# Kernel tuning notes

Measured on AMD Instinct MI355X. Metric: run time of the kernel, lower is better.

## Reference

```python
import jax, jax.numpy as jnp
import numpy as np

KERNEL = 7  # median blur window size (odd)


def setup_inputs() -> dict:
    key = jax.random.key(0)
    # NCHW image batch, values in [0,1) like normalized images
    img = jax.random.uniform(key, (8, 3, 512, 512), dtype=jnp.float32)
    return {"img": img}


def _median_blur(img, k):
    # Matches kornia.filters.median_blur: zero padding ('same'), then median
    # over the k*k window. k*k is odd so the exact middle of the sorted
    # window equals torch.median's lower median.
    pad = k // 2
    b, c, h, w = img.shape
    x = jnp.pad(img, ((0, 0), (0, 0), (pad, pad), (pad, pad)))  # zero pad
    # unfold: [B, C, k*k, H, W] — same materialization as kornia's conv2d
    # with binary one-hot kernels. Loop is over the fixed k*k = 49 taps.
    patches = jnp.stack(
        [x[:, :, i:i + h, j:j + w] for i in range(k) for j in range(k)],
        axis=2,
    )
    mid = (k * k) // 2
    return jnp.sort(patches, axis=2)[:, :, mid]  # [B, C, H, W]


def reference(img):
    return _median_blur(img, KERNEL)
```

## Files before the change

### kernel.cpp

```cpp
#include <hip/hip_runtime.h>
#include <utility>

#define IMG_H 512
#define IMG_W 512

typedef _Float16 h2 __attribute__((ext_vector_type(2)));

__device__ __forceinline__ h2 h2min(h2 a, h2 b) { return __builtin_elementwise_min(a, b); }
__device__ __forceinline__ h2 h2max(h2 a, h2 b) { return __builtin_elementwise_max(a, b); }

struct Op { int kind, a, b; };
constexpr int NSLOT = 352;
constexpr int MAXOPS = 4096;
struct Prog { Op ops[MAXOPS]; int n; int nphys; bool ok; };

constexpr int pow2ceil(int x) { int p = 1; while (p < x) p += p; return p; }

struct Builder {
    Op ops[MAXOPS] = {};
    int n = 0;
    bool pad[NSLOT] = {};
    bool init[NSLOT] = {};
    bool ok = true;

    constexpr void emit(int k, int a, int b) {
        if (n < MAXOPS) ops[n++] = Op{k, a, b}; else ok = false;
    }
    constexpr void load(int s, int c) { emit(2, s, c); pad[s] = false; init[s] = true; }
    constexpr void mov(int d, int s) {
        if (!init[s] || d == s) ok = false;
        emit(1, d, s); pad[d] = pad[s]; init[d] = true;
    }
    constexpr void mkpad(int s) { pad[s] = true; init[s] = true; }
    constexpr void ce_(int a, int b) {
        if (!init[a] || !init[b]) { ok = false; return; }
        if (pad[a] && pad[b]) return;
        if (!pad[a] && pad[b]) return;
        if (pad[a] && !pad[b]) {
            emit(1, a, b); pad[a] = false; pad[b] = true; return;
        }
        emit(0, a, b);
    }
    constexpr void maxin(int a, int b) {
        if (!init[a] || !init[b] || pad[a] || pad[b]) ok = false;
        emit(5, a, b);
    }
    constexpr void minin(int a, int b) {
        if (!init[a] || !init[b] || pad[a] || pad[b]) ok = false;
        emit(4, a, b);
    }
    constexpr void sort_run(int base, int len) {
        for (int p = 1; p < len; p += p)
            for (int k = p; k > 0; k /= 2)
                for (int j = k % p; j + k < len; j += k + k)
                    for (int i = 0; i < k; ++i)
                        if (i + j + k < len)
                            if ((i + j) / (p + p) == (i + j + k) / (p + p))
                                ce_(base + i + j, base + i + j + k);
    }
    constexpr void merge_stage(int base, int P) {
        int nn = 2 * P, p = P;
        for (int k = p; k > 0; k /= 2)
            for (int j = k % p; j + k < nn; j += k + k)
                for (int i = 0; i < k; ++i) {
                    int a = i + j, b = i + j + k;
                    if (b < nn && a / (p + p) == b / (p + p)) ce_(base + a, base + b);
                }
    }
    constexpr void load_col(int base, int c) {
        for (int r = 0; r < 7; ++r) load(base + r, c * 7 + r);
        sort_run(base, 7);
    }
    constexpr void place(int dst, int src, int len, int P) {
        for (int i = 0; i < len; ++i) mov(dst + i, src + i);
        for (int i = len; i < P; ++i) mkpad(dst + i);
    }
    constexpr void merge_to(int dst, int s1, int l1, int s2, int l2) {
        int P = pow2ceil(l1 > l2 ? l1 : l2);
        place(dst, s1, l1, P);
        place(dst + P, s2, l2, P);
        merge_stage(dst, P);
    }
    constexpr void select_med49(int T, int A, int B, int o) {
        for (int t = 0; t < 7; ++t) {
            mov(T + t, A + 17 + t);
            maxin(B + 6 - t, T + t);
        }
        mov(T + 7, A + 24);
        minin(T, T + 1); minin(T + 2, T + 3);
        minin(T + 4, T + 5); minin(T + 6, T + 7);
        minin(T, T + 2); minin(T + 4, T + 6);
        minin(T, T + 4);
        if (!init[T] || pad[T]) ok = false;
        emit(3, o, T);
    }
};

constexpr Prog build() {
    Builder b{};
    constexpr int M12 = 112, M34 = 128, M56 = 144, M78 = 160, M910 = 176, M1112 = 192;
    constexpr int C28A = 208, C28B = 240, C42 = 272, T0 = 336, T1 = 344;

    for (int c = 1; c <= 8; ++c) b.load_col(8 * c, c);
    b.merge_to(M34, 8 * 3, 7, 8 * 4, 7);
    b.merge_to(M56, 8 * 5, 7, 8 * 6, 7);
    b.merge_to(C28A, M34, 14, M56, 14);
    b.merge_to(M12, 8 * 1, 7, 8 * 2, 7);
    b.merge_to(M78, 8 * 7, 7, 8 * 8, 7);

    b.merge_to(C42, C28A, 28, M12, 14);
    b.load_col(8 * 0, 0);
    b.select_med49(T0, C42, 8 * 0, 0);
    b.select_med49(T1, C42, 8 * 7, 1);

    b.merge_to(C42, C28A, 28, M78, 14);
    b.load_col(8 * 9, 9);
    b.select_med49(T0, C42, 8 * 2, 2);
    b.select_med49(T1, C42, 8 * 9, 3);

    b.load_col(8 * 10, 10);
    b.merge_to(M910, 8 * 9, 7, 8 * 10, 7);
    b.merge_to(C28B, M78, 14, M910, 14);

    b.merge_to(C42, C28B, 28, M56, 14);
    b.select_med49(T0, C42, 8 * 4, 4);
    b.load_col(8 * 11, 11);
    b.select_med49(T1, C42, 8 * 11, 5);

    b.load_col(8 * 12, 12);
    b.merge_to(M1112, 8 * 11, 7, 8 * 12, 7);
    b.merge_to(C42, C28B, 28, M1112, 14);
    b.select_med49(T0, C42, 8 * 6, 6);
    b.load_col(8 * 13, 13);
    b.select_med49(T1, C42, 8 * 13, 7);

    Prog p{};
    bool needed[NSLOT] = {};
    int kindr[MAXOPS] = {};
    bool keep[MAXOPS] = {};
    for (int t = b.n - 1; t >= 0; --t) {
        Op o = b.ops[t];
        if (o.kind == 3) { keep[t] = true; kindr[t] = 3; needed[o.b] = true; }
        else if (o.kind == 0) {
            bool na = needed[o.a], nb = needed[o.b];
            if (na && nb)      { keep[t] = true; kindr[t] = 0; }
            else if (na)       { keep[t] = true; kindr[t] = 4; needed[o.b] = true; }
            else if (nb)       { keep[t] = true; kindr[t] = 5; needed[o.a] = true; }
        } else if (o.kind == 1) {
            if (needed[o.a]) { keep[t] = true; kindr[t] = 1; needed[o.a] = false; needed[o.b] = true; }
        } else if (o.kind == 2) {
            if (needed[o.a]) { keep[t] = true; kindr[t] = 2; needed[o.a] = false; }
        } else if (o.kind == 4) {
            if (needed[o.a]) { keep[t] = true; kindr[t] = 4; needed[o.b] = true; }
        } else if (o.kind == 5) {
            if (needed[o.b]) { keep[t] = true; kindr[t] = 5; needed[o.a] = true; }
        }
    }
    p.n = 0;
    for (int t = 0; t < b.n; ++t)
        if (keep[t]) { p.ops[p.n] = b.ops[t]; p.ops[p.n].kind = kindr[t]; ++p.n; }
    p.ok = b.ok;

    bool live[NSLOT] = {};
    bool lu_a[MAXOPS] = {};
    bool lu_b[MAXOPS] = {};
    for (int t = p.n - 1; t >= 0; --t) {
        Op o = p.ops[t];
        if (o.kind == 0 || o.kind == 4 || o.kind == 5) {
            lu_a[t] = !live[o.a]; lu_b[t] = !live[o.b];
        } else if (o.kind == 1 || o.kind == 3) {
            lu_b[t] = !live[o.b];
        }
        if (o.kind == 0) { live[o.a] = false; live[o.b] = false; }
        else if (o.kind == 1 || o.kind == 2 || o.kind == 4) live[o.a] = false;
        else if (o.kind == 5) live[o.b] = false;
        if (o.kind == 0 || o.kind == 4 || o.kind == 5) { live[o.a] = true; live[o.b] = true; }
        else if (o.kind == 1 || o.kind == 3) live[o.b] = true;
    }
    for (int t = 0; t < p.n; ++t) {
        Op o = p.ops[t];
        if (o.kind == 0 && (lu_a[t] || lu_b[t])) p.ok = false;
        if (o.kind == 4 && lu_a[t]) p.ok = false;
        if (o.kind == 5 && lu_b[t]) p.ok = false;
    }
    int phys[NSLOT] = {};
    bool bound[NSLOT] = {};
    int freelist[NSLOT] = {};
    int nfree = 0, nphys = 0;
    for (int t = 0; t < p.n; ++t) {
        Op o = p.ops[t];
        if (o.kind == 0) {
            if (!bound[o.a] || !bound[o.b]) p.ok = false;
            p.ops[t].a = phys[o.a]; p.ops[t].b = phys[o.b];
        } else if (o.kind == 4) {
            if (!bound[o.a] || !bound[o.b]) p.ok = false;
            p.ops[t].a = phys[o.a]; p.ops[t].b = phys[o.b];
            if (lu_b[t]) { freelist[nfree++] = phys[o.b]; bound[o.b] = false; }
        } else if (o.kind == 5) {
            if (!bound[o.a] || !bound[o.b]) p.ok = false;
            p.ops[t].a = phys[o.a]; p.ops[t].b = phys[o.b];
            if (lu_a[t]) { freelist[nfree++] = phys[o.a]; bound[o.a] = false; }
        } else if (o.kind == 1) {
            if (!bound[o.b]) p.ok = false;
            int pb = phys[o.b];
            p.ops[t].b = pb;
            if (lu_b[t]) { freelist[nfree++] = pb; bound[o.b] = false; }
            if (bound[o.a]) { freelist[nfree++] = phys[o.a]; bound[o.a] = false; }
            int pa = (nfree > 0) ? freelist[--nfree] : nphys++;
            phys[o.a] = pa; bound[o.a] = true;
            p.ops[t].a = pa;
        } else if (o.kind == 2) {
            if (bound[o.a]) { freelist[nfree++] = phys[o.a]; bound[o.a] = false; }
            int pa = (nfree > 0) ? freelist[--nfree] : nphys++;
            phys[o.a] = pa; bound[o.a] = true;
            p.ops[t].a = pa;
        } else {
            if (!bound[o.b]) p.ok = false;
            p.ops[t].b = phys[o.b];
            if (lu_b[t]) { freelist[nfree++] = phys[o.b]; bound[o.b] = false; }
        }
        if (nphys > NSLOT || nfree > NSLOT) p.ok = false;
    }
    p.nphys = nphys;
    return p;
}

constexpr Prog PROG = build();
static_assert(PROG.ok && PROG.n > 0 && PROG.n < 2000, "program build failed");
static_assert(PROG.nphys > 0 && PROG.nphys <= 176, "regalloc blew up");
constexpr int NPHYS = PROG.nphys;

template <int I>
__device__ __forceinline__ void step(h2* v, const h2* cols, h2* med) {
    constexpr Op o = PROG.ops[I];
    if constexpr (o.kind == 0) {
        h2 lo = h2min(v[o.a], v[o.b]);
        h2 hi = h2max(v[o.a], v[o.b]);
        v[o.a] = lo; v[o.b] = hi;
    } else if constexpr (o.kind == 1) v[o.a] = v[o.b];
    else if constexpr (o.kind == 2) v[o.a] = cols[o.b];
    else if constexpr (o.kind == 3) med[o.a] = v[o.b];
    else if constexpr (o.kind == 4) v[o.a] = h2min(v[o.a], v[o.b]);
    else v[o.b] = h2max(v[o.a], v[o.b]);
}

template <size_t... Is>
__device__ __forceinline__ void run_all(h2* v, const h2* cols, h2* med,
                                        std::index_sequence<Is...>) {
    (step<(int)Is>(v, cols, med), ...);
}

__global__ __launch_bounds__(256, 2) void median7x7_kernel(
        const float* __restrict__ img, float* __restrict__ out) {
    const int bc = blockIdx.z;
    const int tx = threadIdx.x;
    const int ty = threadIdx.y;
    const int x0 = (blockIdx.x * 64 + tx) * 8;
    const int y  = (blockIdx.y * 4 + ty) * 2;

    const float* base = img + (size_t)bc * (IMG_H * IMG_W);
    const bool okl = (x0 >= 4);
    const bool okr = (x0 <= 496);
    const int xl = okl ? (x0 - 4) : 0;
    const int xr = okr ? (x0 + 8) : 504;

    h2 colv[98];
    float prv[14];
#pragma unroll
    for (int r = 0; r < 8; ++r) {
        const int yy = y - 3 + r;
        float4 Q0, Q1, Q2, Q3;
        if ((unsigned)yy < IMG_H) {
            const float* rp = base + (size_t)yy * IMG_W;
            Q0 = *(const float4*)(rp + xl);
            Q1 = *(const float4*)(rp + x0);
            Q2 = *(const float4*)(rp + x0 + 4);
            Q3 = *(const float4*)(rp + xr);
        } else {
            Q0 = make_float4(0.f, 0.f, 0.f, 0.f); Q1 = Q0; Q2 = Q0; Q3 = Q0;
        }
        float cur[14];
        cur[0] = okl ? Q0.y : 0.f; cur[1] = okl ? Q0.z : 0.f; cur[2] = okl ? Q0.w : 0.f;
        cur[3] = Q1.x; cur[4] = Q1.y; cur[5] = Q1.z; cur[6] = Q1.w;
        cur[7] = Q2.x; cur[8] = Q2.y; cur[9] = Q2.z; cur[10] = Q2.w;
        cur[11] = okr ? Q3.x : 0.f; cur[12] = okr ? Q3.y : 0.f; cur[13] = okr ? Q3.z : 0.f;
        if (r > 0) {
#pragma unroll
            for (int c = 0; c < 14; ++c)
                colv[c * 7 + (r - 1)] = (h2)__builtin_amdgcn_cvt_pkrtz(prv[c], cur[c]);
        }
#pragma unroll
        for (int c = 0; c < 14; ++c) prv[c] = cur[c];
    }

    h2 v[NPHYS];
    h2 med[8];
    run_all(v, colv, med, std::make_index_sequence<(size_t)PROG.n>{});

    float* op = out + (size_t)bc * (IMG_H * IMG_W) + (size_t)y * IMG_W + x0;
    *(float4*)op = make_float4((float)med[0].x, (float)med[1].x,
                               (float)med[2].x, (float)med[3].x);
    *(float4*)(op + 4) = make_float4((float)med[4].x, (float)med[5].x,
                                     (float)med[6].x, (float)med[7].x);
    *(float4*)(op + IMG_W) = make_float4((float)med[0].y, (float)med[1].y,
                                         (float)med[2].y, (float)med[3].y);
    *(float4*)(op + IMG_W + 4) = make_float4((float)med[4].y, (float)med[5].y,
                                             (float)med[6].y, (float)med[7].y);
}

extern "C" void kernel_launch(void* const* d_in, const int* in_sizes, int n_in,
                              void* d_out, int out_size, void* d_ws, size_t ws_size,
                              hipStream_t stream) {
    const float* img = (const float*)d_in[0];
    float* out = (float*)d_out;
    dim3 grid(1, 64, 24);
    dim3 block(64, 4, 1);
    hipLaunchKernelGGL(median7x7_kernel, grid, block, 0, stream, img, out);
}
```

Before: 88.79 us.

## Halve per-thread output width from 8 to 4 columns and double the grid

Each thread now produces a 4-wide by 2-tall output tile instead of 8 by 2, so the sorting-network program only computes 4 medians, loads 10 columns and keeps fewer values live. The grid doubles in x to cover the image. This is meant to cut register pressure and raise parallelism. The cost is less reuse of the shared merged columns (the C28 sorted block is amortized over fewer outputs) and more redundant loads and merges per output pixel.

```diff
diff --git a/kernel.cpp b/kernel.cpp
--- a/kernel.cpp
+++ b/kernel.cpp
@@ -98,8 +98,8 @@
 
 constexpr Prog build() {
     Builder b{};
-    constexpr int M12 = 112, M34 = 128, M56 = 144, M78 = 160, M910 = 176, M1112 = 192;
-    constexpr int C28A = 208, C28B = 240, C42 = 272, T0 = 336, T1 = 344;
+    constexpr int M12 = 112, M34 = 128, M56 = 144, M78 = 160;
+    constexpr int C28A = 208, C42 = 272, T0 = 336, T1 = 344;
 
     for (int c = 1; c <= 8; ++c) b.load_col(8 * c, c);
     b.merge_to(M34, 8 * 3, 7, 8 * 4, 7);
@@ -117,22 +117,6 @@
     b.load_col(8 * 9, 9);
     b.select_med49(T0, C42, 8 * 2, 2);
     b.select_med49(T1, C42, 8 * 9, 3);
-
-    b.load_col(8 * 10, 10);
-    b.merge_to(M910, 8 * 9, 7, 8 * 10, 7);
-    b.merge_to(C28B, M78, 14, M910, 14);
-
-    b.merge_to(C42, C28B, 28, M56, 14);
-    b.select_med49(T0, C42, 8 * 4, 4);
-    b.load_col(8 * 11, 11);
-    b.select_med49(T1, C42, 8 * 11, 5);
-
-    b.load_col(8 * 12, 12);
-    b.merge_to(M1112, 8 * 11, 7, 8 * 12, 7);
-    b.merge_to(C42, C28B, 28, M1112, 14);
-    b.select_med49(T0, C42, 8 * 6, 6);
-    b.load_col(8 * 13, 13);
-    b.select_med49(T1, C42, 8 * 13, 7);
 
     Prog p{};
     bool needed[NSLOT] = {};
@@ -255,57 +239,51 @@
     const int bc = blockIdx.z;
     const int tx = threadIdx.x;
     const int ty = threadIdx.y;
-    const int x0 = (blockIdx.x * 64 + tx) * 8;
+    const int x0 = (blockIdx.x * 64 + tx) * 4;
     const int y  = (blockIdx.y * 4 + ty) * 2;
 
     const float* base = img + (size_t)bc * (IMG_H * IMG_W);
     const bool okl = (x0 >= 4);
-    const bool okr = (x0 <= 496);
+    const bool okr = (x0 <= 504);
     const int xl = okl ? (x0 - 4) : 0;
-    const int xr = okr ? (x0 + 8) : 504;
-
-    h2 colv[98];
-    float prv[14];
+    const int xr = okr ? (x0 + 4) : 504;
+
+    h2 colv[70];
+    float prv[10];
 #pragma unroll
     for (int r = 0; r < 8; ++r) {
         const int yy = y - 3 + r;
-        float4 Q0, Q1, Q2, Q3;
+        float4 Q0, Q1, Q2;
         if ((unsigned)yy < IMG_H) {
             const float* rp = base + (size_t)yy * IMG_W;
             Q0 = *(const float4*)(rp + xl);
             Q1 = *(const float4*)(rp + x0);
-            Q2 = *(const float4*)(rp + x0 + 4);
-            Q3 = *(const float4*)(rp + xr);
+            Q2 = *(const float4*)(rp + xr);
         } else {
-            Q0 = make_float4(0.f, 0.f, 0.f, 0.f); Q1 = Q0; Q2 = Q0; Q3 = Q0;
-        }
-        float cur[14];
+            Q0 = make_float4(0.f, 0.f, 0.f, 0.f); Q1 = Q0; Q2 = Q0;
+        }
+        float cur[10];
         cur[0] = okl ? Q0.y : 0.f; cur[1] = okl ? Q0.z : 0.f; cur[2] = okl ? Q0.w : 0.f;
         cur[3] = Q1.x; cur[4] = Q1.y; cur[5] = Q1.z; cur[6] = Q1.w;
-        cur[7] = Q2.x; cur[8] = Q2.y; cur[9] = Q2.z; cur[10] = Q2.w;
-        cur[11] = okr ? Q3.x : 0.f; cur[12] = okr ? Q3.y : 0.f; cur[13] = okr ? Q3.z : 0.f;
+        cur[7] = okr ? Q2.x : 0.f; cur[8] = okr ? Q2.y : 0.f; cur[9] = okr ? Q2.z : 0.f;
         if (r > 0) {
 #pragma unroll
-            for (int c = 0; c < 14; ++c)
+            for (int c = 0; c < 10; ++c)
                 colv[c * 7 + (r - 1)] = (h2)__builtin_amdgcn_cvt_pkrtz(prv[c], cur[c]);
         }
 #pragma unroll
-        for (int c = 0; c < 14; ++c) prv[c] = cur[c];
+        for (int c = 0; c < 10; ++c) prv[c] = cur[c];
     }
 
     h2 v[NPHYS];
-    h2 med[8];
+    h2 med[4];
     run_all(v, colv, med, std::make_index_sequence<(size_t)PROG.n>{});
 
     float* op = out + (size_t)bc * (IMG_H * IMG_W) + (size_t)y * IMG_W + x0;
     *(float4*)op = make_float4((float)med[0].x, (float)med[1].x,
                                (float)med[2].x, (float)med[3].x);
-    *(float4*)(op + 4) = make_float4((float)med[4].x, (float)med[5].x,
-                                     (float)med[6].x, (float)med[7].x);
     *(float4*)(op + IMG_W) = make_float4((float)med[0].y, (float)med[1].y,
                                          (float)med[2].y, (float)med[3].y);
-    *(float4*)(op + IMG_W + 4) = make_float4((float)med[4].y, (float)med[5].y,
-                                             (float)med[6].y, (float)med[7].y);
 }
 
 extern "C" void kernel_launch(void* const* d_in, const int* in_sizes, int n_in,
@@ -313,7 +291,7 @@
                               hipStream_t stream) {
     const float* img = (const float*)d_in[0];
     float* out = (float*)d_out;
-    dim3 grid(1, 64, 24);
+    dim3 grid(2, 64, 24);
     dim3 block(64, 4, 1);
     hipLaunchKernelGGL(median7x7_kernel, grid, block, 0, stream, img, out);
 }
```

New measurement: 94.07 us. 1.06x slower.
